# Kernel tuning notes

Measured on AMD Instinct MI355X. Metric: run time of the kernel, lower is better.

## Reference

```python
import jax, jax.numpy as jnp
import numpy as np

N_GAS_NETS = 76  # 29 h2o + 13 o3 + 9 co2 + 3 n2o + 9 ch4 + 13 uniform
N_CHANNELS = 29
N_IN = 2   # (temperature, pressure)
H = 64     # hidden width per n_hidden=[64,64]

# gas index (into composition[0..5]) for each of the 76 stacked nets
COMP_IDX = jnp.asarray(np.repeat(np.arange(6), [29, 13, 9, 3, 9, 13]))

# sparse per-channel combine (hard-coded in the original forward)
H2O_IDX = jnp.asarray([0,1,2,3,4,5,6,3,4,9,10,11,12,13,14,15,16,17,18,19,20,21,22,23,24,25,26,27,28])
O3_CH  = jnp.asarray([0,1,2,17,18,19,20,21,22,25,26,27,28])
CO2_CH = jnp.asarray([0,1,2,5,6,9,10,13,14])
N2O_CH = jnp.asarray([0,1,2])
CH4_CH = jnp.asarray([0,1,2,3,4,7,8,11,12])
U_CH   = jnp.asarray([0,1,2,15,16,17,18,19,20,21,22,27,28])


def setup_inputs() -> dict:
    key = jax.random.key(0)
    ks = jax.random.split(key, 10)
    N = 32768
    t_p = jax.random.normal(ks[0], (N, N_IN), dtype=jnp.float32)
    composition = jax.random.uniform(ks[1], (8, N, 1), dtype=jnp.float32)
    s1 = 1.0 / np.sqrt(N_IN)
    s2 = 1.0 / np.sqrt(H)
    W1 = jax.random.normal(ks[2], (N_GAS_NETS, N_IN, H), dtype=jnp.float32) * s1
    b1 = jnp.zeros((N_GAS_NETS, H), dtype=jnp.float32)
    W2 = jax.random.normal(ks[3], (N_GAS_NETS, H, H), dtype=jnp.float32) * s2
    b2 = jnp.zeros((N_GAS_NETS, H), dtype=jnp.float32)
    Wout = jax.random.normal(ks[4], (N_GAS_NETS, H, 1), dtype=jnp.float32) * s2
    bout = jnp.zeros((N_GAS_NETS, 1), dtype=jnp.float32)
    ke_lw = jax.random.uniform(ks[5], (N_CHANNELS, 1), dtype=jnp.float32)
    ke_iw = jax.random.uniform(ks[6], (N_CHANNELS, 1), dtype=jnp.float32)
    return {"t_p": t_p, "composition": composition, "W1": W1, "b1": b1,
            "W2": W2, "b2": b2, "Wout": Wout, "bout": bout,
            "ke_lw": ke_lw, "ke_iw": ke_iw}


def reference(t_p, composition, W1, b1, W2, b2, Wout, bout, ke_lw, ke_iw):
    # Batched evaluation of all 76 tiny DenseFFN experts on the shared t_p input.
    h = jax.nn.relu(jnp.einsum('ni,gih->gnh', t_p, W1) + b1[:, None, :])   # [76,N,H]
    h = jax.nn.relu(jnp.einsum('gnh,ghk->gnk', h, W2) + b2[:, None, :])    # [76,N,H]
    ke = jax.nn.relu(jnp.einsum('gnh,gho->gno', h, Wout) + bout[:, None, :])  # [76,N,1]

    # tau_gas[gas] = ke * composition[gas_index]
    tau_all = ke * composition[COMP_IDX]  # [76,N,1]
    h2o = tau_all[0:29]
    o3 = tau_all[29:42]
    co2 = tau_all[42:51]
    n2o = tau_all[51:54]
    ch4 = tau_all[54:63]
    u = tau_all[63:76]

    # hard-coded sparse per-channel sum
    tau_gases = h2o[H2O_IDX]                      # [29,N,1]
    tau_gases = tau_gases.at[O3_CH].add(o3)
    tau_gases = tau_gases.at[CO2_CH].add(co2)
    tau_gases = tau_gases.at[N2O_CH].add(n2o)
    tau_gases = tau_gases.at[CH4_CH].add(ch4)
    tau_gases = tau_gases.at[U_CH].add(u)

    tau_lw = ke_lw[:, None, :] * composition[6]   # [29,N,1]
    tau_iw = ke_iw[:, None, :] * composition[7]   # [29,N,1]
    return (tau_gases, tau_lw, tau_iw)
```

## Files before the change

kernel.cpp:

```cpp
#include <hip/hip_runtime.h>

#define NPTS 32768

typedef _Float16 f16;
typedef _Float16 f16x2 __attribute__((ext_vector_type(2)));
typedef _Float16 f16x8 __attribute__((ext_vector_type(8)));
typedef float f32x2 __attribute__((ext_vector_type(2)));
typedef float f32x4 __attribute__((ext_vector_type(4)));

union H8 { f16x8 v8; f16x2 v2[4]; };

static __device__ __forceinline__ f16x2 pk_fma(f16x2 a, f16x2 b, f16x2 c) {
  return __builtin_elementwise_fma(a, b, c);
}
static __device__ __forceinline__ f16x2 pk_relu(f16x2 a) {
  f16x2 z = {(f16)0.f, (f16)0.f};
  return __builtin_elementwise_max(a, z);
}
static __device__ __forceinline__ f16x2 pk_cvt(float a, float b) {
  return __builtin_bit_cast(f16x2, __builtin_amdgcn_cvt_pkrtz(a, b));
}

__device__ const unsigned char G_T[74] = {
  0,0,0,0,0,0,0, 0,0,0,0,0,0,0,0,0,0,0,0,0,0,0,0,0,0,0,0,
  1,1,1,1,1,1,1,1,1,1,1,1,1,
  2,2,2,2,2,2,2,2,2,
  3,3,3,
  4,4,4,4,4,4,4,4,4,
  5,5,5,5,5,5,5,5,5,5,5,5,5
};
__device__ const unsigned char G_C1[74] = {
  0,1,2,3,4,5,6, 9,10,11,12,13,14,15,16,17,18,19,20,21,22,23,24,25,26,27,28,
  0,1,2,17,18,19,20,21,22,25,26,27,28,
  0,1,2,5,6,9,10,13,14,
  0,1,2,
  0,1,2,3,4,7,8,11,12,
  0,1,2,15,16,17,18,19,20,21,22,27,28
};
__device__ const unsigned char G_C2[74] = {
  255,255,255,7,8,255,255, 255,255,255,255,255,255,255,255,255,255,255,255,
  255,255,255,255,255,255,255,255,
  255,255,255,255,255,255,255,255,255,255,255,255,255,
  255,255,255,255,255,255,255,255,255,
  255,255,255,
  255,255,255,255,255,255,255,255,255,
  255,255,255,255,255,255,255,255,255,255,255,255,255
};

__global__ __launch_bounds__(256) void k0_init(
    const float* __restrict__ comp, const float* __restrict__ ke_lw,
    const float* __restrict__ ke_iw, float* __restrict__ out)
{
  const int c = blockIdx.x >> 7;
  const int n = ((blockIdx.x & 127) << 8) + threadIdx.x;
  out[c * NPTS + n] = 0.f;
  out[29 * NPTS + c * NPTS + n] = ke_lw[c] * comp[6 * NPTS + n];
  out[58 * NPTS + c * NPTS + n] = ke_iw[c] * comp[7 * NPTS + n];
}

__global__ __launch_bounds__(256, 2) void k1_mlp(
    const float* __restrict__ t_p, const float* __restrict__ comp,
    const float* __restrict__ W1, const float* __restrict__ b1,
    const float* __restrict__ W2, const float* __restrict__ b2,
    const float* __restrict__ Wout, const float* __restrict__ bout,
    float* __restrict__ out)
{
  const int lane = threadIdx.x & 63;
  const int l15  = lane & 15;
  const int quad = lane >> 4;
  const int w    = blockIdx.x * 4 + (threadIdx.x >> 6);
  const int gi   = w >> 8;
  const int g    = gi + (gi >= 7 ? 2 : 0);
  const int pb0  = (w & 255) * 128;

  const int t  = G_T[gi];
  const int c1 = G_C1[gi];
  const int c2 = G_C2[gi];

  const bool qb0 = (quad & 1) != 0;
  const bool qb1 = (quad & 2) != 0;

  H8 afrag[4][2];
  const float* W2g = W2 + g * 4096;
  #pragma unroll
  for (int mt = 0; mt < 4; ++mt) {
    #pragma unroll
    for (int ks = 0; ks < 2; ++ks) {
      const float* src = W2g + (ks * 32 + quad * 8) * 64 + mt * 16 + l15;
      #pragma unroll
      for (int i = 0; i < 4; ++i)
        afrag[mt][ks].v2[i] = pk_cvt(src[(2 * i) * 64], src[(2 * i + 1) * 64]);
    }
  }

  f16x2 w0h[2][4], w1h[2][4], b1h[2][4];
  const float* W1g = W1 + g * 128;
  const float* b1g = b1 + g * 64;
  #pragma unroll
  for (int ks = 0; ks < 2; ++ks) {
    #pragma unroll
    for (int i = 0; i < 4; ++i) {
      int h = ks * 32 + quad * 8 + 2 * i;
      w0h[ks][i] = pk_cvt(W1g[h],      W1g[h + 1]);
      w1h[ks][i] = pk_cvt(W1g[64 + h], W1g[64 + h + 1]);
      b1h[ks][i] = pk_cvt(b1g[h],      b1g[h + 1]);
    }
  }

  f32x4 b2q[4];
  f32x2 wq2[4][2];
  #pragma unroll
  for (int mt = 0; mt < 4; ++mt) {
    b2q[mt] = *(const f32x4*)(b2 + g * 64 + mt * 16 + quad * 4);
    f32x4 wv = *(const f32x4*)(Wout + g * 64 + mt * 16 + quad * 4);
    wq2[mt][0] = f32x2{ wv[0], wv[1] };
    wq2[mt][1] = f32x2{ wv[2], wv[3] };
  }
  const float bo = bout[g];

  const float2* tp2 = (const float2*)t_p;
  const float* compt = comp + t * NPTS;
  float* out1 = out + c1 * NPTS;
  float* out2 = (c2 == 255) ? nullptr : out + c2 * NPTS;

  #pragma unroll
  for (int pass = 0; pass < 2; ++pass) {
    const int pb = pb0 + pass * 64;

    float2 xv[4];
    #pragma unroll
    for (int pt = 0; pt < 4; ++pt)
      xv[pt] = tp2[pb + pt * 16 + l15];
    const float cv = compt[pb + lane];

    f16x2 x0v[4], x1v[4];
    #pragma unroll
    for (int pt = 0; pt < 4; ++pt) {
      x0v[pt] = pk_cvt(xv[pt].x, xv[pt].x);
      x1v[pt] = pk_cvt(xv[pt].y, xv[pt].y);
    }

    H8 bfrag[2][4];
    #pragma unroll
    for (int ks = 0; ks < 2; ++ks)
      #pragma unroll
      for (int pt = 0; pt < 4; ++pt)
        #pragma unroll
        for (int i = 0; i < 4; ++i)
          bfrag[ks][pt].v2[i] =
              pk_relu(pk_fma(x0v[pt], w0h[ks][i], pk_fma(x1v[pt], w1h[ks][i], b1h[ks][i])));

    f32x4 acc[4][4];
    #pragma unroll
    for (int mt = 0; mt < 4; ++mt)
      #pragma unroll
      for (int pt = 0; pt < 4; ++pt) {
        f32x4 c0 = __builtin_amdgcn_mfma_f32_16x16x32_f16(
            afrag[mt][0].v8, bfrag[0][pt].v8, b2q[mt], 0, 0, 0);
        acc[mt][pt] = __builtin_amdgcn_mfma_f32_16x16x32_f16(
            afrag[mt][1].v8, bfrag[1][pt].v8, c0, 0, 0, 0);
      }

    float p[4];
    #pragma unroll
    for (int pt = 0; pt < 4; ++pt) {
      f32x2 p2 = { 0.f, 0.f };
      #pragma unroll
      for (int mt = 0; mt < 4; ++mt) {
        f32x2 z = { 0.f, 0.f };
        f32x2 a0 = { acc[mt][pt][0], acc[mt][pt][1] };
        f32x2 a1 = { acc[mt][pt][2], acc[mt][pt][3] };
        a0 = __builtin_elementwise_max(a0, z);
        a1 = __builtin_elementwise_max(a1, z);
        p2 = __builtin_elementwise_fma(a0, wq2[mt][0], p2);
        p2 = __builtin_elementwise_fma(a1, wq2[mt][1], p2);
      }
      p[pt] = p2[0] + p2[1];
    }

    float u = qb1 ? (qb0 ? p[3] : p[2]) : (qb0 ? p[1] : p[0]);
    float v = qb1 ? (qb0 ? p[2] : p[3]) : (qb0 ? p[0] : p[1]);
    float wv2 = qb1 ? (qb0 ? p[1] : p[0]) : (qb0 ? p[3] : p[2]);
    float x = qb1 ? (qb0 ? p[0] : p[1]) : (qb0 ? p[2] : p[3]);
    float s = u + __shfl_xor(v, 16, 64);
    float tt = wv2 + __shfl_xor(x, 16, 64);
    float r = s + __shfl_xor(tt, 32, 64);

    float tau = fmaxf(r + bo, 0.f) * cv;
    atomicAdd(&out1[pb + lane], tau);
    if (out2) atomicAdd(&out2[pb + lane], tau);
  }
}

extern "C" void kernel_launch(void* const* d_in, const int* in_sizes, int n_in,
                              void* d_out, int out_size, void* d_ws, size_t ws_size,
                              hipStream_t stream)
{
  const float* t_p   = (const float*)d_in[0];
  const float* comp  = (const float*)d_in[1];
  const float* W1    = (const float*)d_in[2];
  const float* b1    = (const float*)d_in[3];
  const float* W2    = (const float*)d_in[4];
  const float* b2    = (const float*)d_in[5];
  const float* Wout  = (const float*)d_in[6];
  const float* bout  = (const float*)d_in[7];
  const float* ke_lw = (const float*)d_in[8];
  const float* ke_iw = (const float*)d_in[9];
  float* out = (float*)d_out;

  k0_init<<<29 * 128, 256, 0, stream>>>(comp, ke_lw, ke_iw, out);
  k1_mlp<<<4736, 256, 0, stream>>>(t_p, comp, W1, b1, W2, b2, Wout, bout, out);
}
```

Measured before the change: 121.2 us.

## Pre-pack fp16 weight fragments per expert and amortize over more points per wave

```diff
diff --git a/kernel.cpp b/kernel.cpp
--- a/kernel.cpp
+++ b/kernel.cpp
@@ -7,8 +7,9 @@
 typedef _Float16 f16x8 __attribute__((ext_vector_type(8)));
 typedef float f32x2 __attribute__((ext_vector_type(2)));
 typedef float f32x4 __attribute__((ext_vector_type(4)));
-
-union H8 { f16x8 v8; f16x2 v2[4]; };
+typedef unsigned int u32x4 __attribute__((ext_vector_type(4)));
+
+union U16 { u32x4 u; f32x4 f; f16x2 h2[4]; f16x8 h8; };
 
 static __device__ __forceinline__ f16x2 pk_fma(f16x2 a, f16x2 b, f16x2 c) {
   return __builtin_elementwise_fma(a, b, c);
@@ -47,6 +48,60 @@
   255,255,255,255,255,255,255,255,255,255,255,255,255
 };
 
+#define NSLOT 22
+
+__global__ __launch_bounds__(64) void k0w_pack(
+    const float* __restrict__ W1, const float* __restrict__ b1,
+    const float* __restrict__ W2, const float* __restrict__ b2,
+    const float* __restrict__ Wout, u32x4* __restrict__ pack)
+{
+  const int gi   = blockIdx.x;
+  const int lane = threadIdx.x;
+  const int l15  = lane & 15;
+  const int quad = lane >> 4;
+  const int g    = gi + (gi >= 7 ? 2 : 0);
+
+  const float* W2g = W2 + g * 4096;
+  const float* W1g = W1 + g * 128;
+  const float* b1g = b1 + g * 64;
+  u32x4* dst = pack + gi * NSLOT * 64 + lane;
+
+  #pragma unroll
+  for (int mt = 0; mt < 4; ++mt)
+    #pragma unroll
+    for (int ks = 0; ks < 2; ++ks) {
+      U16 u;
+      #pragma unroll
+      for (int j = 0; j < 4; ++j) {
+        const float* s = W2g + (ks * 32 + quad * 8 + 2 * j) * 64 + mt * 16 + l15;
+        u.h2[j] = pk_cvt(s[0], s[64]);
+      }
+      dst[(mt * 2 + ks) * 64] = u.u;
+    }
+  #pragma unroll
+  for (int ks = 0; ks < 2; ++ks) {
+    U16 a, b, c;
+    #pragma unroll
+    for (int j = 0; j < 4; ++j) {
+      int h = ks * 32 + quad * 8 + 2 * j;
+      a.h2[j] = pk_cvt(W1g[h],      W1g[h + 1]);
+      b.h2[j] = pk_cvt(W1g[64 + h], W1g[64 + h + 1]);
+      c.h2[j] = pk_cvt(b1g[h],      b1g[h + 1]);
+    }
+    dst[(8 + ks) * 64]  = a.u;
+    dst[(10 + ks) * 64] = b.u;
+    dst[(12 + ks) * 64] = c.u;
+  }
+  #pragma unroll
+  for (int mt = 0; mt < 4; ++mt) {
+    U16 u, v;
+    u.f = *(const f32x4*)(b2   + g * 64 + mt * 16 + quad * 4);
+    v.f = *(const f32x4*)(Wout + g * 64 + mt * 16 + quad * 4);
+    dst[(14 + mt) * 64] = u.u;
+    dst[(18 + mt) * 64] = v.u;
+  }
+}
+
 __global__ __launch_bounds__(256) void k0_init(
     const float* __restrict__ comp, const float* __restrict__ ke_lw,
     const float* __restrict__ ke_iw, float* __restrict__ out)
@@ -58,20 +113,18 @@
   out[58 * NPTS + c * NPTS + n] = ke_iw[c] * comp[7 * NPTS + n];
 }
 
-__global__ __launch_bounds__(256, 2) void k1_mlp(
+__global__ __launch_bounds__(256, 4) void k1_mlp(
     const float* __restrict__ t_p, const float* __restrict__ comp,
-    const float* __restrict__ W1, const float* __restrict__ b1,
-    const float* __restrict__ W2, const float* __restrict__ b2,
-    const float* __restrict__ Wout, const float* __restrict__ bout,
+    const u32x4* __restrict__ pack, const float* __restrict__ bout,
     float* __restrict__ out)
 {
   const int lane = threadIdx.x & 63;
   const int l15  = lane & 15;
   const int quad = lane >> 4;
   const int w    = blockIdx.x * 4 + (threadIdx.x >> 6);
-  const int gi   = w >> 8;
+  const int gi   = w >> 6;
   const int g    = gi + (gi >= 7 ? 2 : 0);
-  const int pb0  = (w & 255) * 128;
+  const int pb0  = (w & 63) * 512;
 
   const int t  = G_T[gi];
   const int c1 = G_C1[gi];
@@ -80,42 +133,32 @@
   const bool qb0 = (quad & 1) != 0;
   const bool qb1 = (quad & 2) != 0;
 
-  H8 afrag[4][2];
-  const float* W2g = W2 + g * 4096;
-  #pragma unroll
-  for (int mt = 0; mt < 4; ++mt) {
-    #pragma unroll
-    for (int ks = 0; ks < 2; ++ks) {
-      const float* src = W2g + (ks * 32 + quad * 8) * 64 + mt * 16 + l15;
-      #pragma unroll
-      for (int i = 0; i < 4; ++i)
-        afrag[mt][ks].v2[i] = pk_cvt(src[(2 * i) * 64], src[(2 * i + 1) * 64]);
-    }
-  }
-
-  f16x2 w0h[2][4], w1h[2][4], b1h[2][4];
-  const float* W1g = W1 + g * 128;
-  const float* b1g = b1 + g * 64;
-  #pragma unroll
-  for (int ks = 0; ks < 2; ++ks) {
-    #pragma unroll
-    for (int i = 0; i < 4; ++i) {
-      int h = ks * 32 + quad * 8 + 2 * i;
-      w0h[ks][i] = pk_cvt(W1g[h],      W1g[h + 1]);
-      w1h[ks][i] = pk_cvt(W1g[64 + h], W1g[64 + h + 1]);
-      b1h[ks][i] = pk_cvt(b1g[h],      b1g[h + 1]);
-    }
-  }
-
+  const u32x4* pksrc = pack + gi * NSLOT * 64 + lane;
+  U16 slot[NSLOT];
+  #pragma unroll
+  for (int i = 0; i < NSLOT; ++i)
+    slot[i].u = pksrc[i * 64];
+
+  f16x8 afrag[4][2];
   f32x4 b2q[4];
   f32x2 wq2[4][2];
   #pragma unroll
   for (int mt = 0; mt < 4; ++mt) {
-    b2q[mt] = *(const f32x4*)(b2 + g * 64 + mt * 16 + quad * 4);
-    f32x4 wv = *(const f32x4*)(Wout + g * 64 + mt * 16 + quad * 4);
-    wq2[mt][0] = f32x2{ wv[0], wv[1] };
-    wq2[mt][1] = f32x2{ wv[2], wv[3] };
-  }
+    afrag[mt][0] = slot[mt * 2 + 0].h8;
+    afrag[mt][1] = slot[mt * 2 + 1].h8;
+    b2q[mt] = slot[14 + mt].f;
+    wq2[mt][0] = f32x2{ slot[18 + mt].f[0], slot[18 + mt].f[1] };
+    wq2[mt][1] = f32x2{ slot[18 + mt].f[2], slot[18 + mt].f[3] };
+  }
+  f16x2 w0h[2][4], w1h[2][4], b1h[2][4];
+  #pragma unroll
+  for (int ks = 0; ks < 2; ++ks)
+    #pragma unroll
+    for (int j = 0; j < 4; ++j) {
+      w0h[ks][j] = slot[8 + ks].h2[j];
+      w1h[ks][j] = slot[10 + ks].h2[j];
+      b1h[ks][j] = slot[12 + ks].h2[j];
+    }
   const float bo = bout[g];
 
   const float2* tp2 = (const float2*)t_p;
@@ -123,8 +166,7 @@
   float* out1 = out + c1 * NPTS;
   float* out2 = (c2 == 255) ? nullptr : out + c2 * NPTS;
 
-  #pragma unroll
-  for (int pass = 0; pass < 2; ++pass) {
+  for (int pass = 0; pass < 8; ++pass) {
     const int pb = pb0 + pass * 64;
 
     float2 xv[4];
@@ -140,51 +182,54 @@
       x1v[pt] = pk_cvt(xv[pt].y, xv[pt].y);
     }
 
-    H8 bfrag[2][4];
+    U16 bfrag[2][4];
     #pragma unroll
     for (int ks = 0; ks < 2; ++ks)
       #pragma unroll
       for (int pt = 0; pt < 4; ++pt)
         #pragma unroll
         for (int i = 0; i < 4; ++i)
-          bfrag[ks][pt].v2[i] =
+          bfrag[ks][pt].h2[i] =
               pk_relu(pk_fma(x0v[pt], w0h[ks][i], pk_fma(x1v[pt], w1h[ks][i], b1h[ks][i])));
 
-    f32x4 acc[4][4];
-    #pragma unroll
-    for (int mt = 0; mt < 4; ++mt)
+    f32x2 p2[4];
+    #pragma unroll
+    for (int pt = 0; pt < 4; ++pt) p2[pt] = f32x2{ 0.f, 0.f };
+
+    #pragma unroll
+    for (int mt = 0; mt < 4; ++mt) {
+      f32x4 c[4];
+      #pragma unroll
+      for (int pt = 0; pt < 4; ++pt)
+        c[pt] = __builtin_amdgcn_mfma_f32_16x16x32_f16(
+            afrag[mt][0], bfrag[0][pt].h8, b2q[mt], 0, 0, 0);
+      #pragma unroll
+      for (int pt = 0; pt < 4; ++pt)
+        c[pt] = __builtin_amdgcn_mfma_f32_16x16x32_f16(
+            afrag[mt][1], bfrag[1][pt].h8, c[pt], 0, 0, 0);
       #pragma unroll
       for (int pt = 0; pt < 4; ++pt) {
-        f32x4 c0 = __builtin_amdgcn_mfma_f32_16x16x32_f16(
-            afrag[mt][0].v8, bfrag[0][pt].v8, b2q[mt], 0, 0, 0);
-        acc[mt][pt] = __builtin_amdgcn_mfma_f32_16x16x32_f16(
-            afrag[mt][1].v8, bfrag[1][pt].v8, c0, 0, 0, 0);
-      }
-
-    float p[4];
-    #pragma unroll
-    for (int pt = 0; pt < 4; ++pt) {
-      f32x2 p2 = { 0.f, 0.f };
-      #pragma unroll
-      for (int mt = 0; mt < 4; ++mt) {
         f32x2 z = { 0.f, 0.f };
-        f32x2 a0 = { acc[mt][pt][0], acc[mt][pt][1] };
-        f32x2 a1 = { acc[mt][pt][2], acc[mt][pt][3] };
+        f32x2 a0 = { c[pt][0], c[pt][1] };
+        f32x2 a1 = { c[pt][2], c[pt][3] };
         a0 = __builtin_elementwise_max(a0, z);
         a1 = __builtin_elementwise_max(a1, z);
-        p2 = __builtin_elementwise_fma(a0, wq2[mt][0], p2);
-        p2 = __builtin_elementwise_fma(a1, wq2[mt][1], p2);
+        p2[pt] = __builtin_elementwise_fma(a0, wq2[mt][0], p2[pt]);
+        p2[pt] = __builtin_elementwise_fma(a1, wq2[mt][1], p2[pt]);
       }
-      p[pt] = p2[0] + p2[1];
-    }
-
-    float u = qb1 ? (qb0 ? p[3] : p[2]) : (qb0 ? p[1] : p[0]);
-    float v = qb1 ? (qb0 ? p[2] : p[3]) : (qb0 ? p[0] : p[1]);
-    float wv2 = qb1 ? (qb0 ? p[1] : p[0]) : (qb0 ? p[3] : p[2]);
-    float x = qb1 ? (qb0 ? p[0] : p[1]) : (qb0 ? p[2] : p[3]);
-    float s = u + __shfl_xor(v, 16, 64);
-    float tt = wv2 + __shfl_xor(x, 16, 64);
-    float r = s + __shfl_xor(tt, 32, 64);
+    }
+
+    float p[4];
+    #pragma unroll
+    for (int pt = 0; pt < 4; ++pt) p[pt] = p2[pt][0] + p2[pt][1];
+
+    float u  = qb1 ? (qb0 ? p[3] : p[2]) : (qb0 ? p[1] : p[0]);
+    float v  = qb1 ? (qb0 ? p[2] : p[3]) : (qb0 ? p[0] : p[1]);
+    float w2 = qb1 ? (qb0 ? p[1] : p[0]) : (qb0 ? p[3] : p[2]);
+    float x  = qb1 ? (qb0 ? p[0] : p[1]) : (qb0 ? p[2] : p[3]);
+    float s  = u + __shfl_xor(v, 16, 64);
+    float tt = w2 + __shfl_xor(x, 16, 64);
+    float r  = s + __shfl_xor(tt, 32, 64);
 
     float tau = fmaxf(r + bo, 0.f) * cv;
     atomicAdd(&out1[pb + lane], tau);
@@ -207,7 +252,9 @@
   const float* ke_lw = (const float*)d_in[8];
   const float* ke_iw = (const float*)d_in[9];
   float* out = (float*)d_out;
-
+  u32x4* pack = (u32x4*)d_ws;
+
+  k0w_pack<<<74, 64, 0, stream>>>(W1, b1, W2, b2, Wout, pack);
   k0_init<<<29 * 128, 256, 0, stream>>>(comp, ke_lw, ke_iw, out);
-  k1_mlp<<<4736, 256, 0, stream>>>(t_p, comp, W1, b1, W2, b2, Wout, bout, out);
-}
+  k1_mlp<<<1184, 256, 0, stream>>>(t_p, comp, pack, bout, out);
+}
```

Result: slower. 156.9 us (+29.5%).
